# Optimization experiments

Measured on AMD Instinct MI355X. Metric: run time of the kernel, lower is better.

The kernel has to match this reference:

```python
import jax, jax.numpy as jnp
import numpy as np

N, L, WD, PD, FS, NF, C = 1024, 128, 300, 50, 3, 512, 53
V, PV = 100000, 256          # word vocab, position-feature vocab
D = WD + 2 * PD              # 400: concat token representation width
LP = L - FS + 1              # 126: conv output length (valid conv)
NEG = jnp.float32(-1e30)


def setup_inputs() -> dict:
    key = jax.random.key(0)
    ks = jax.random.split(key, 11)
    tokens = jax.random.randint(ks[0], (N, L), 0, V, dtype=jnp.int32)
    pf1 = jax.random.randint(ks[1], (N, L), 0, PV, dtype=jnp.int32)
    pf2 = jax.random.randint(ks[2], (N, L), 0, PV, dtype=jnp.int32)
    # entity positions in conv-output coordinates, sorted so p1 <= p2 < LP
    entity_pos = jnp.sort(jax.random.randint(ks[3], (N, 2), 0, LP, dtype=jnp.int32), axis=1)
    wordvec = jax.random.normal(ks[4], (V, WD), jnp.float32) * 0.02
    pf1_emb = jax.random.normal(ks[5], (PV, PD), jnp.float32) * 0.02
    pf2_emb = jax.random.normal(ks[6], (PV, PD), jnp.float32) * 0.02
    conv_w = jax.random.normal(ks[7], (NF, FS, D), jnp.float32) * (1.0 / np.sqrt(FS * D))
    conv_b = jnp.zeros((NF,), jnp.float32)
    out_w = jax.random.normal(ks[8], (3 * NF, C), jnp.float32) * (1.0 / np.sqrt(3 * NF))
    out_b = jnp.zeros((C,), jnp.float32)
    return dict(tokens=tokens, pf1=pf1, pf2=pf2, entity_pos=entity_pos,
                wordvec=wordvec, pf1_emb=pf1_emb, pf2_emb=pf2_emb,
                conv_w=conv_w, conv_b=conv_b, out_w=out_w, out_b=out_b)


def reference(tokens, pf1, pf2, entity_pos, wordvec, pf1_emb, pf2_emb,
              conv_w, conv_b, out_w, out_b):
    # token representation: [N, L, D]
    x = jnp.concatenate([wordvec[tokens], pf1_emb[pf1], pf2_emb[pf2]], axis=-1)
    # valid conv over seq with kernel spanning full feature width -> matmul form
    win = jnp.stack([x[:, k:k + LP, :] for k in range(FS)], axis=2)  # [N, LP, FS, D]
    conv = jnp.tanh(jnp.einsum('ntkd,fkd->ntf', win, conv_w) + conv_b)  # [N, LP, NF]
    # piecewise (3-segment) max pool keyed on entity positions
    idx = jnp.arange(LP)[None, :]                      # [1, LP]
    p1 = entity_pos[:, 0:1]                            # [N, 1]
    p2 = entity_pos[:, 1:2]
    m1 = idx <= p1                                     # [0, p1]
    m2 = (idx >= p1) & (idx <= p2)                     # [p1, p2]
    m3 = idx >= p2                                     # [p2, LP)
    masks = jnp.stack([m1, m2, m3], axis=1)            # [N, 3, LP]
    pooled = jnp.max(jnp.where(masks[:, :, :, None], conv[:, None, :, :], NEG), axis=2)  # [N, 3, NF]
    # torch code: cat(pool1,pool2,pool3) -> [3,F], transpose -> [F,3], flatten
    feat = jnp.transpose(pooled, (0, 2, 1)).reshape(N, 3 * NF)  # [N, 3*NF]
    return feat @ out_w + out_b                        # [N, C]
```

## Files before the change

kernel.cpp:

```cpp
#include <hip/hip_runtime.h>


#define XSTRIDE 424
#define LPV 126
#define NC 53

typedef __attribute__((ext_vector_type(8))) short short8;
typedef __attribute__((ext_vector_type(4))) float floatx4;

__device__ __forceinline__ unsigned short f2bf_rne(float x) {
    unsigned u = __float_as_uint(x);
    u += 0x7fffu + ((u >> 16) & 1u);
    return (unsigned short)(u >> 16);
}

__global__ void __launch_bounds__(1024)
prep(const float* __restrict__ convw, const float* __restrict__ outw,
     unsigned short* __restrict__ convwb2, float* __restrict__ outwT) {
    int i = blockIdx.x * 1024 + threadIdx.x;
    if (i < 622592) {
        int e = i & 7, col = (i >> 3) & 15, kq = (i >> 7) & 3;
        int rest = i >> 9;
        int ks = rest % 38, ftile = rest / 38;
        int k = ks * 32 + kq * 8 + e, f = ftile * 16 + col;
        convwb2[i] = (k < 1200) ? f2bf_rne(convw[f * 1200 + k])
                                : (unsigned short)0;
    } else {
        int i2 = i - 622592;
        if (i2 < 81408) {
            int c = i2 / 1536, j = i2 - c * 1536;
            outwT[i2] = outw[j * 53 + c];
        }
    }
}

extern "C" __global__ void __launch_bounds__(512, 4)
pcnn_half(const int* __restrict__ tokens, const int* __restrict__ pf1,
          const int* __restrict__ pf2, const int* __restrict__ epos,
          const float* __restrict__ wordvec,
          const float* __restrict__ pf1e,
          const float* __restrict__ pf2e,
          const unsigned short* __restrict__ convwb2,
          float* __restrict__ pfe)
{
    extern __shared__ char smem[];
    unsigned short* xl = (unsigned short*)smem;
    int* idx = (int*)(smem + 56816);

    const int bid = blockIdx.x;
    const int n   = bid >> 1;
    const int wr  = bid & 1;
    const int r0  = wr * 64;
    const int nreal = wr ? 64 : 67;

    const int tid  = threadIdx.x;
    const int lane = tid & 63;
    const int wv   = tid >> 6;

    if (tid < nreal) {
        int base = n * 128 + r0 + tid;
        idx[tid]       = tokens[base];
        idx[67 + tid]  = pf1[base];
        idx[134 + tid] = pf2[base];
    }
    if (wr) {
        const short8 z8 = {0, 0, 0, 0, 0, 0, 0, 0};
        short8* dst = (short8*)xl;
        for (int i = tid; i < 159; i += 512) {
            int row = 64 + i / 53, c = i % 53;
            dst[row * 53 + c] = z8;
        }
    }
    __syncthreads();

    {
        const float4* wv4 = (const float4*)wordvec;
        const float2* p12 = (const float2*)pf1e;
        const float2* p22 = (const float2*)pf2e;
        #pragma unroll 4
        for (int i = tid; i < nreal * 75; i += 512) {
            int row = i / 75, c = i - row * 75;
            float4 v = wv4[(long)idx[row] * 75 + c];
            *(ushort4*)(xl + row * XSTRIDE + 4 * c) =
                make_ushort4(f2bf_rne(v.x), f2bf_rne(v.y),
                             f2bf_rne(v.z), f2bf_rne(v.w));
        }
        #pragma unroll 4
        for (int i = tid; i < nreal * 25; i += 512) {
            int row = i / 25, c = i - row * 25;
            float2 v = p12[idx[67 + row] * 25 + c];
            *(ushort2*)(xl + row * XSTRIDE + 300 + 2 * c) =
                make_ushort2(f2bf_rne(v.x), f2bf_rne(v.y));
            float2 w = p22[idx[134 + row] * 25 + c];
            *(ushort2*)(xl + row * XSTRIDE + 350 + 2 * c) =
                make_ushort2(f2bf_rne(w.x), f2bf_rne(w.y));
        }
    }
    __syncthreads();

    const int col = lane & 15;
    const int kq  = lane >> 4;

    const floatx4 fz = {0.f, 0.f, 0.f, 0.f};
    floatx4 acc[4][4];
    #pragma unroll
    for (int mt = 0; mt < 4; ++mt)
        #pragma unroll
        for (int jt = 0; jt < 4; ++jt) acc[mt][jt] = fz;

    int ck   = kq * 8;
    int aoff = col * XSTRIDE + kq * 8;
    const unsigned short* bb = convwb2 + lane * 8;

    #pragma unroll 1
    for (int ks = 0; ks < 38; ++ks) {
        short8 b[4], a[4];
        #pragma unroll
        for (int jt = 0; jt < 4; ++jt)
            b[jt] = *(const short8*)(bb + ((wv * 4 + jt) * 38 + ks) * 512);
        #pragma unroll
        for (int mt = 0; mt < 4; ++mt)
            a[mt] = *(const short8*)(xl + aoff + mt * (16 * XSTRIDE));
        __builtin_amdgcn_s_setprio(1);
        #pragma unroll
        for (int mt = 0; mt < 4; ++mt)
            #pragma unroll
            for (int jt = 0; jt < 4; ++jt)
                acc[mt][jt] = __builtin_amdgcn_mfma_f32_16x16x32_bf16(
                    a[mt], b[jt], acc[mt][jt], 0, 0, 0);
        __builtin_amdgcn_s_setprio(0);
        ck += 32; aoff += 32;
        if (ck >= 400) { ck -= 400; aoff += XSTRIDE - 400; }
    }

    const int p1 = epos[2 * n], p2 = epos[2 * n + 1];
    float* pf_out = pfe + (n * 2 + wr) * 1536;
    #pragma unroll
    for (int jt = 0; jt < 4; ++jt) {
        float m0 = -1e30f, m1 = -1e30f, m2 = -1e30f;
        #pragma unroll
        for (int mt = 0; mt < 4; ++mt) {
            #pragma unroll
            for (int r = 0; r < 4; ++r) {
                int gt = r0 + mt * 16 + kq * 4 + r;
                float v = acc[mt][jt][r];
                if (gt < LPV) {
                    if (gt <= p1) m0 = fmaxf(m0, v);
                    if (gt >= p1 && gt <= p2) m1 = fmaxf(m1, v);
                    if (gt >= p2) m2 = fmaxf(m2, v);
                }
            }
        }
        m0 = fmaxf(m0, __shfl_xor(m0, 16)); m0 = fmaxf(m0, __shfl_xor(m0, 32));
        m1 = fmaxf(m1, __shfl_xor(m1, 16)); m1 = fmaxf(m1, __shfl_xor(m1, 32));
        m2 = fmaxf(m2, __shfl_xor(m2, 16)); m2 = fmaxf(m2, __shfl_xor(m2, 32));
        if (kq == 0) {
            int f = wv * 64 + jt * 16 + col;
            pf_out[3 * f + 0] = m0;
            pf_out[3 * f + 1] = m1;
            pf_out[3 * f + 2] = m2;
        }
    }
}

extern "C" __global__ void __launch_bounds__(256)
pcnn_out(const float* __restrict__ pfe, const float* __restrict__ convb,
         const float* __restrict__ outwT,
         const float* __restrict__ outb, float* __restrict__ out)
{
    __shared__ float feat[1536];
    const int n = blockIdx.x;
    const int tid = threadIdx.x;
    const float* pa = pfe + n * 3072;
    const float* pb = pa + 1536;

    for (int i = tid; i < 1536; i += 256) {
        float v = fmaxf(pa[i], pb[i]);
        feat[i] = tanhf(v + convb[i / 3]);
    }
    __syncthreads();

    const int lane = tid & 63;
    const int wv   = tid >> 6;
    for (int cc = wv; cc < NC; cc += 4) {
        const float* wrow = outwT + cc * 1536;
        float s = 0.f;
        #pragma unroll 4
        for (int jj = lane; jj < 1536; jj += 64)
            s += feat[jj] * wrow[jj];
        s += __shfl_xor(s, 32); s += __shfl_xor(s, 16);
        s += __shfl_xor(s, 8);  s += __shfl_xor(s, 4);
        s += __shfl_xor(s, 2);  s += __shfl_xor(s, 1);
        if (lane == 0) out[n * 53 + cc] = s + outb[cc];
    }
}

extern "C" void kernel_launch(void* const* d_in, const int* in_sizes, int n_in,
                              void* d_out, int out_size, void* d_ws, size_t ws_size,
                              hipStream_t stream) {
    (void)in_sizes; (void)n_in; (void)ws_size; (void)out_size;
    const int* tokens = (const int*)d_in[0];
    const int* pf1    = (const int*)d_in[1];
    const int* pf2    = (const int*)d_in[2];
    const int* epos   = (const int*)d_in[3];
    const float* wordvec = (const float*)d_in[4];
    const float* pf1e    = (const float*)d_in[5];
    const float* pf2e    = (const float*)d_in[6];
    const float* convw   = (const float*)d_in[7];
    const float* convb   = (const float*)d_in[8];
    const float* outw    = (const float*)d_in[9];
    const float* outb    = (const float*)d_in[10];
    float* out = (float*)d_out;

    unsigned short* convwb2 = (unsigned short*)d_ws;
    float* outwT = (float*)((char*)d_ws + 1245184);
    float* pfe   = (float*)((char*)d_ws + 1570816);

    prep<<<dim3(688), dim3(1024), 0, stream>>>(convw, outw, convwb2, outwT);

    const size_t lds_bytes = 56816 + 816;
    pcnn_half<<<dim3(2048), dim3(512), lds_bytes, stream>>>(
        tokens, pf1, pf2, epos, wordvec, pf1e, pf2e, convwb2, pfe);

    pcnn_out<<<dim3(1024), dim3(256), 0, stream>>>(pfe, convb, outwT, outb, out);
}
```

Measured before the change: 362.4 us.

## Stagger K-loop start per wave and batch eight samples per output block

In the conv kernel, each wave starts its K loop at an offset that depends on the wave and block index and wraps around. This spreads the waves across different weight slices and LDS addresses, to reduce contention on the same cache lines and banks. The output kernel now handles eight samples per block and keeps each weight row in registers for reuse across them, which cuts outwT reloads eightfold. The cost is fewer blocks in the output kernel (128), an 8x larger LDS footprint there, and extra index bookkeeping in the MFMA loop.

```diff
diff --git a/kernel.cpp b/kernel.cpp
--- a/kernel.cpp
+++ b/kernel.cpp
@@ -108,16 +108,19 @@
         #pragma unroll
         for (int jt = 0; jt < 4; ++jt) acc[mt][jt] = fz;
 
-    int ck   = kq * 8;
-    int aoff = col * XSTRIDE + kq * 8;
-    const unsigned short* bb = convwb2 + lane * 8;
-
+    const int ks0 = (wv * 5 + bid % 19) % 38;
+    const int kb  = ks0 * 32 + kq * 8;
+    int ck   = kb % 400;
+    int aoff = (col + kb / 400) * XSTRIDE + ck;
+    const unsigned short* bwv = convwb2 + (wv * 4 * 38) * 512 + lane * 8;
+
+    int ks = ks0;
     #pragma unroll 1
-    for (int ks = 0; ks < 38; ++ks) {
+    for (int i = 0; i < 38; ++i) {
         short8 b[4], a[4];
         #pragma unroll
         for (int jt = 0; jt < 4; ++jt)
-            b[jt] = *(const short8*)(bb + ((wv * 4 + jt) * 38 + ks) * 512);
+            b[jt] = *(const short8*)(bwv + (jt * 38 + ks) * 512);
         #pragma unroll
         for (int mt = 0; mt < 4; ++mt)
             a[mt] = *(const short8*)(xl + aoff + mt * (16 * XSTRIDE));
@@ -129,8 +132,9 @@
                 acc[mt][jt] = __builtin_amdgcn_mfma_f32_16x16x32_bf16(
                     a[mt], b[jt], acc[mt][jt], 0, 0, 0);
         __builtin_amdgcn_s_setprio(0);
-        ck += 32; aoff += 32;
+        ++ks; ck += 32; aoff += 32;
         if (ck >= 400) { ck -= 400; aoff += XSTRIDE - 400; }
+        if (ks == 38) { ks = 0; ck = kq * 8; aoff = col * XSTRIDE + ck; }
     }
 
     const int p1 = epos[2 * n], p2 = epos[2 * n + 1];
@@ -168,30 +172,38 @@
          const float* __restrict__ outwT,
          const float* __restrict__ outb, float* __restrict__ out)
 {
-    __shared__ float feat[1536];
-    const int n = blockIdx.x;
+    __shared__ float feat[8 * 1536];
+    const int n0 = blockIdx.x * 8;
     const int tid = threadIdx.x;
-    const float* pa = pfe + n * 3072;
-    const float* pb = pa + 1536;
-
-    for (int i = tid; i < 1536; i += 256) {
-        float v = fmaxf(pa[i], pb[i]);
-        feat[i] = tanhf(v + convb[i / 3]);
+
+    #pragma unroll 1
+    for (int nl = 0; nl < 8; ++nl) {
+        const float* pa = pfe + (n0 + nl) * 3072;
+        for (int j = tid; j < 1536; j += 256) {
+            float v = fmaxf(pa[j], pa[1536 + j]);
+            feat[nl * 1536 + j] = tanhf(v + convb[j / 3]);
+        }
     }
     __syncthreads();
 
     const int lane = tid & 63;
     const int wv   = tid >> 6;
     for (int cc = wv; cc < NC; cc += 4) {
-        const float* wrow = outwT + cc * 1536;
-        float s = 0.f;
-        #pragma unroll 4
-        for (int jj = lane; jj < 1536; jj += 64)
-            s += feat[jj] * wrow[jj];
-        s += __shfl_xor(s, 32); s += __shfl_xor(s, 16);
-        s += __shfl_xor(s, 8);  s += __shfl_xor(s, 4);
-        s += __shfl_xor(s, 2);  s += __shfl_xor(s, 1);
-        if (lane == 0) out[n * 53 + cc] = s + outb[cc];
+        float wrow[24];
+        const float* wp = outwT + cc * 1536 + lane;
+        #pragma unroll
+        for (int u = 0; u < 24; ++u) wrow[u] = wp[u * 64];
+        #pragma unroll 1
+        for (int nl = 0; nl < 8; ++nl) {
+            const float* fp = feat + nl * 1536 + lane;
+            float s = 0.f;
+            #pragma unroll
+            for (int u = 0; u < 24; ++u) s += fp[u * 64] * wrow[u];
+            s += __shfl_xor(s, 32); s += __shfl_xor(s, 16);
+            s += __shfl_xor(s, 8);  s += __shfl_xor(s, 4);
+            s += __shfl_xor(s, 2);  s += __shfl_xor(s, 1);
+            if (lane == 0) out[(n0 + nl) * 53 + cc] = s + outb[cc];
+        }
     }
 }
 
@@ -222,5 +234,5 @@
     pcnn_half<<<dim3(2048), dim3(512), lds_bytes, stream>>>(
         tokens, pf1, pf2, epos, wordvec, pf1e, pf2e, convwb2, pfe);
 
-    pcnn_out<<<dim3(1024), dim3(256), 0, stream>>>(pfe, convb, outwT, outb, out);
-}
+    pcnn_out<<<dim3(128), dim3(256), 0, stream>>>(pfe, convb, outwT, outb, out);
+}
```

Result: slower. 403.8 us (+11.4%).
